# Performance work log

Measured on AMD Instinct MI355X. Metric: run time of the kernel, lower is better.

Reference implementation:

```python
import jax, jax.numpy as jnp
import numpy as np

NEG_INF = -1e9


def setup_inputs() -> dict:
    key = jax.random.key(0)
    ks = jax.random.split(key, 6)
    B, S, E, D = 32, 2048, 1024, 1024
    dec_hidden = jax.random.normal(ks[0], (B, D), dtype=jnp.float32)
    enc_outputs = jax.random.normal(ks[1], (B, S, E), dtype=jnp.float32)
    mask = jax.random.randint(ks[2], (B, S), 0, 2, dtype=jnp.int32)
    # scale weights ~ Glorot-ish so tanh isn't saturated
    W_enc = jax.random.normal(ks[3], (D, E), dtype=jnp.float32) / np.sqrt(E)
    W_dec = jax.random.normal(ks[4], (D, D), dtype=jnp.float32) / np.sqrt(D)
    v = jax.random.normal(ks[5], (D,), dtype=jnp.float32) / np.sqrt(D)
    return {"dec_hidden": dec_hidden, "enc_outputs": enc_outputs, "mask": mask,
            "W_enc": W_enc, "W_dec": W_dec, "v": v}


def reference(dec_hidden, enc_outputs, mask, W_enc, W_dec, v):
    # dh: [B, D]  (torch Linear: x @ W.T)
    dh = dec_hidden @ W_dec.T
    # eh: [B, S, D]
    eh = jnp.einsum('bse,de->bsd', enc_outputs, W_enc)
    # additive energy + projection by v -> scores [B, S]
    energy = jnp.tanh(dh[:, None, :] + eh)
    scores = jnp.einsum('bsd,d->bs', energy, v)
    scores = jnp.where(mask == 0, NEG_INF, scores)
    weights = jax.nn.softmax(scores, axis=1)          # [B, S]
    context = jnp.einsum('bs,bse->be', weights, enc_outputs)  # [B, E]
    return context, weights
```

## Files before the change

### kernel.cpp

```cpp
#include <hip/hip_runtime.h>
#include <stdint.h>

typedef float f32x4 __attribute__((ext_vector_type(4)));
typedef float f32x16 __attribute__((ext_vector_type(16)));
typedef short bf16x8 __attribute__((ext_vector_type(8)));
typedef unsigned short ushort8 __attribute__((ext_vector_type(8)));

__device__ __forceinline__ unsigned short f2bf(float x) {
  union { float f; uint32_t u; } c; c.f = x;
  return (unsigned short)((c.u + 0x8000u) >> 16);
}
__device__ __forceinline__ float bf2f(unsigned short u) {
  union { uint32_t u; float f; } c; c.u = ((uint32_t)u) << 16;
  return c.f;
}


__global__ void prep_fused_k(const float* __restrict__ W, unsigned short* __restrict__ Wt,
                             const float* __restrict__ dec, const float* __restrict__ Wd,
                             float* __restrict__ dh) {
  if (blockIdx.x < 512) {
    int t = blockIdx.x * 256 + threadIdx.x;
    int d  = t >> 7;
    int c0 = (t & 127) << 3;
    const float* src = W + ((size_t)d << 10) + c0;
    f32x4 f0 = *(const f32x4*)src;
    f32x4 f1 = *(const f32x4*)(src + 4);
    ushort8 u;
    u[0]=f2bf(f0[0]); u[1]=f2bf(f0[1]); u[2]=f2bf(f0[2]); u[3]=f2bf(f0[3]);
    u[4]=f2bf(f1[0]); u[5]=f2bf(f1[1]); u[6]=f2bf(f1[2]); u[7]=f2bf(f1[3]);
    int nt = d >> 7, r = d & 127;
    int kt = c0 >> 6, kb = (c0 & 63) >> 3;
    *(ushort8*)(Wt + ((size_t)nt << 17) + (kt << 13) + ((kb * 128 + r) << 3)) = u;
  } else {
    __shared__ float sdec[1024];
    int bb = blockIdx.x - 512;
    int b = bb >> 2;
    for (int i = threadIdx.x; i < 1024; i += 256) sdec[i] = dec[(b << 10) + i];
    __syncthreads();
    int d = ((bb & 3) << 8) + threadIdx.x;
    const float* wr = Wd + ((size_t)d << 10);
    float a = 0.f;
    for (int k = 0; k < 1024; k += 4) {
      f32x4 wv = *(const f32x4*)(wr + k);
      f32x4 xv = *(const f32x4*)(&sdec[k]);
      a += wv[0]*xv[0] + wv[1]*xv[1] + wv[2]*xv[2] + wv[3]*xv[3];
    }
    dh[(b << 10) + d] = a;
  }
}

__global__ void compact_k(const int* __restrict__ mask, int* __restrict__ rows,
                          int* __restrict__ cnt, float* __restrict__ wout) {
  int b = blockIdx.x, tid = threadIdx.x;
  int lane = tid & 63, wv = tid >> 6;
  int mloc[8]; int c = 0;
  #pragma unroll
  for (int ii = 0; ii < 8; ++ii) {
    int s = tid * 8 + ii;
    int m = mask[(b << 11) + s];
    mloc[ii] = m; c += m;
    wout[(b << 11) + s] = 0.f;
  }
  int inc = c;
  #pragma unroll
  for (int off = 1; off < 64; off <<= 1) {
    int nn = __shfl_up(inc, off);
    if (lane >= off) inc += nn;
  }
  __shared__ int wsum[4];
  if (lane == 63) wsum[wv] = inc;
  __syncthreads();
  int base = 0;
  for (int w = 0; w < wv; ++w) base += wsum[w];
  int idx = base + inc - c;
  #pragma unroll
  for (int ii = 0; ii < 8; ++ii) {
    if (mloc[ii]) { rows[(b << 11) + idx] = tid * 8 + ii; ++idx; }
  }
  if (tid == 0) cnt[b] = wsum[0] + wsum[1] + wsum[2] + wsum[3];
}

__global__ void pack8_k(const float* __restrict__ enc, const int* __restrict__ rows,
                        const int* __restrict__ cnt, unsigned short* __restrict__ encP) {
  int b = blockIdx.x >> 4, mt = blockIdx.x & 15;
  int n = cnt[b];
  if (mt * 128 >= n) return;
  __shared__ int sr[128];
  __shared__ unsigned short T[128 * 64];
  int tid = threadIdx.x;
  if (tid < 128) {
    int i = mt * 128 + tid; if (i >= n) i = n - 1;
    sr[tid] = rows[(b << 11) + i];
  }
  __syncthreads();
  unsigned short* dst = encP + (((size_t)(b * 16 + mt)) << 17);
  for (int kt = 0; kt < 16; ++kt) {
    #pragma unroll
    for (int p = 0; p < 4; ++p) {
      int id = p * 256 + tid;
      int r = id >> 3, cseg = id & 7;
      const float* src = enc + (((size_t)(b << 11) + sr[r]) << 10) + (kt << 6) + (cseg << 3);
      f32x4 f0 = *(const f32x4*)src;
      f32x4 f1 = *(const f32x4*)(src + 4);
      ushort8 u;
      u[0]=f2bf(f0[0]); u[1]=f2bf(f0[1]); u[2]=f2bf(f0[2]); u[3]=f2bf(f0[3]);
      u[4]=f2bf(f1[0]); u[5]=f2bf(f1[1]); u[6]=f2bf(f1[2]); u[7]=f2bf(f1[3]);
      *(ushort8*)&T[(r << 6) + ((cseg ^ (r & 7)) << 3)] = u;
    }
    __syncthreads();
    unsigned short* g = dst + (kt << 13);
    #pragma unroll
    for (int p = 0; p < 4; ++p) {
      int blk = p * 256 + tid;
      int kb = blk >> 7, r = blk & 127;
      ushort8 u = *(const ushort8*)&T[(r << 6) + ((kb ^ (r & 7)) << 3)];
      *(ushort8*)(g + (blk << 3)) = u;
    }
    __syncthreads();
  }
}

__global__ __launch_bounds__(256, 4) void score9_k(
    const unsigned short* __restrict__ encP, const unsigned short* __restrict__ Wt,
    const float* __restrict__ dh, const float* __restrict__ v,
    const int* __restrict__ cnt, float* __restrict__ pscores)
{
  int L  = (blockIdx.x & 7) * 512 + (blockIdx.x >> 3);
  int b  = L >> 7, mt = (L >> 3) & 15, nt = L & 7;
  int n  = cnt[b];
  if (mt * 128 >= n) return;

  __shared__ __align__(16) unsigned short AS[2][4096];
  __shared__ __align__(16) unsigned short BS[2][4096];

  int tid  = threadIdx.x;
  int lane = tid & 63;
  int wv   = tid >> 6;
  int wm = wv >> 1, wn = wv & 1;
  int l31 = lane & 31, l5 = lane >> 5;

  const unsigned short* aT = encP + (((size_t)(b * 16 + mt)) << 17);
  const unsigned short* bT = Wt + ((size_t)nt << 17);

  int offA[2][2], offB[2][2];
  #pragma unroll
  for (int mf = 0; mf < 2; ++mf) {
    int r = wm * 64 + mf * 32 + l31;
    #pragma unroll
    for (int ki = 0; ki < 2; ++ki)
      offA[mf][ki] = (((ki * 2 + l5) << 7) + r) << 3;
  }
  #pragma unroll
  for (int nf = 0; nf < 2; ++nf) {
    int r = wn * 64 + nf * 32 + l31;
    #pragma unroll
    for (int ki = 0; ki < 2; ++ki)
      offB[nf][ki] = (((ki * 2 + l5) << 7) + r) << 3;
  }

  f32x16 acc[2][2];
  #pragma unroll
  for (int i = 0; i < 2; ++i)
    #pragma unroll
    for (int j = 0; j < 2; ++j)
      #pragma unroll
      for (int e = 0; e < 16; ++e)
        acc[i][j][e] = 0.f;

  auto stage = [&](int slot, int kt) {
    #pragma unroll
    for (int j = 0; j < 2; ++j) {
      int off = j * 2048 + tid * 8;
      __builtin_amdgcn_global_load_lds(
        (const __attribute__((address_space(1))) void*)(const void*)(aT + ((size_t)kt << 12) + off),
        (__attribute__((address_space(3))) void*)(void*)(&AS[slot][off]), 16, 0, 0);
      __builtin_amdgcn_global_load_lds(
        (const __attribute__((address_space(1))) void*)(const void*)(bT + ((size_t)kt << 12) + off),
        (__attribute__((address_space(3))) void*)(void*)(&BS[slot][off]), 16, 0, 0);
    }
  };

  auto compute = [&](int slot) {
    #pragma unroll
    for (int ki = 0; ki < 2; ++ki) {
      bf16x8 af[2], bf[2];
      #pragma unroll
      for (int mf = 0; mf < 2; ++mf) af[mf] = *(const bf16x8*)&AS[slot][offA[mf][ki]];
      #pragma unroll
      for (int nf = 0; nf < 2; ++nf) bf[nf] = *(const bf16x8*)&BS[slot][offB[nf][ki]];
      #pragma unroll
      for (int mf = 0; mf < 2; ++mf)
        #pragma unroll
        for (int nf = 0; nf < 2; ++nf)
          acc[mf][nf] = __builtin_amdgcn_mfma_f32_32x32x16_bf16(af[mf], bf[nf], acc[mf][nf], 0, 0, 0);
    }
  };

  stage(0, 0);
  __syncthreads();
  int slot = 0;
  for (int kt = 0; kt < 31; ++kt) {
    stage(slot ^ 1, kt + 1);
    compute(slot);
    __syncthreads();
    slot ^= 1;
  }
  compute(slot);

  float* sc = (float*)AS;
  float vv[2], dd[2];
  #pragma unroll
  for (int nf = 0; nf < 2; ++nf) {
    int dcol = nt * 128 + wn * 64 + nf * 32 + l31;
    vv[nf] = v[dcol];
    dd[nf] = dh[(b << 10) + dcol];
  }
  #pragma unroll
  for (int mf = 0; mf < 2; ++mf) {
    #pragma unroll
    for (int reg = 0; reg < 16; ++reg) {
      float p = 0.f;
      #pragma unroll
      for (int nf = 0; nf < 2; ++nf) {
        float x = acc[mf][nf][reg] + dd[nf];
        float e = __expf(2.0f * x);
        float t = 1.0f - __fdividef(2.0f, e + 1.0f);
        p += vv[nf] * t;
      }
      p += __shfl_xor(p, 1); p += __shfl_xor(p, 2); p += __shfl_xor(p, 4);
      p += __shfl_xor(p, 8); p += __shfl_xor(p, 16);
      if (l31 == 0) {
        int row = wm * 64 + mf * 32 + (reg & 3) + 8 * (reg >> 2) + 4 * l5;
        sc[row * 2 + wn] = p;
      }
    }
  }
  __syncthreads();
  if (tid < 128) {
    int i = mt * 128 + tid;
    if (i < n)
      pscores[(((size_t)nt) << 16) + (b << 11) + i] = sc[tid * 2 + 0] + sc[tid * 2 + 1];
  }
}

__global__ void softmax4_k(const float* __restrict__ ps, const int* __restrict__ rows,
                           const int* __restrict__ cnt, float* __restrict__ wout,
                           float* __restrict__ wc) {
  int b = blockIdx.x;
  int tid = threadIdx.x;
  int n = cnt[b];
  float val[8];
  float m = -INFINITY;
  #pragma unroll
  for (int ii = 0; ii < 8; ++ii) {
    int i = tid + ii * 256;
    float s = -INFINITY;
    if (i < n) {
      s = 0.f;
      #pragma unroll
      for (int nt = 0; nt < 8; ++nt) s += ps[(((size_t)nt) << 16) + (b << 11) + i];
    }
    val[ii] = s;
    m = fmaxf(m, s);
  }
  #pragma unroll
  for (int off = 1; off < 64; off <<= 1) m = fmaxf(m, __shfl_xor(m, off));
  __shared__ float r1[4], r2[4];
  if ((tid & 63) == 0) r1[tid >> 6] = m;
  __syncthreads();
  m = fmaxf(fmaxf(r1[0], r1[1]), fmaxf(r1[2], r1[3]));
  float ssum = 0.f;
  #pragma unroll
  for (int ii = 0; ii < 8; ++ii) { val[ii] = __expf(val[ii] - m); ssum += val[ii]; }
  #pragma unroll
  for (int off = 1; off < 64; off <<= 1) ssum += __shfl_xor(ssum, off);
  if ((tid & 63) == 0) r2[tid >> 6] = ssum;
  __syncthreads();
  ssum = r2[0] + r2[1] + r2[2] + r2[3];
  float inv = 1.0f / ssum;
  #pragma unroll
  for (int ii = 0; ii < 8; ++ii) {
    int i = tid + ii * 256;
    if (i < n) {
      float w = val[ii] * inv;
      wc[(b << 11) + i] = w;
      wout[((size_t)b << 11) + rows[(b << 11) + i]] = w;
    }
  }
}

__global__ void ctx8_k(const unsigned short* __restrict__ encP, const float* __restrict__ wc,
                       const int* __restrict__ cnt, float* __restrict__ cp) {
  int b = blockIdx.x >> 4, mt = blockIdx.x & 15;
  int n = cnt[b];
  float* out = cp + (((size_t)(b * 16 + mt)) << 10);
  int tid = threadIdx.x;
  if (mt * 128 >= n) {
    #pragma unroll
    for (int j = 0; j < 4; ++j) out[tid * 4 + j] = 0.f;
    return;
  }
  __shared__ float sw[128];
  __shared__ float red[128][8];
  if (tid < 128) {
    int i = mt * 128 + tid;
    sw[tid] = (i < n) ? wc[(b << 11) + i] : 0.f;
  }
  __syncthreads();
  const unsigned short* tile = encP + (((size_t)(b * 16 + mt)) << 17);
  int cb8  = tid & 127;
  int half = tid >> 7;
  const unsigned short* base = tile + ((cb8 >> 3) << 13) + ((cb8 & 7) << 10);
  float a[8];
  #pragma unroll
  for (int j = 0; j < 8; ++j) a[j] = 0.f;
  for (int rr = 0; rr < 64; ++rr) {
    int r = half * 64 + rr;
    float w = sw[r];
    ushort8 u = *(const ushort8*)(base + (r << 3));
    #pragma unroll
    for (int j = 0; j < 8; ++j) a[j] += w * bf2f(u[j]);
  }
  if (half == 1) {
    #pragma unroll
    for (int j = 0; j < 8; ++j) red[cb8][j] = a[j];
  }
  __syncthreads();
  if (half == 0) {
    #pragma unroll
    for (int j = 0; j < 8; ++j) out[cb8 * 8 + j] = a[j] + red[cb8][j];
  }
}

__global__ void ctx_red4_k(const float* __restrict__ cp, float* __restrict__ out) {
  int t = blockIdx.x * 256 + threadIdx.x;
  int b = t >> 10, e = t & 1023;
  float a = 0.f;
  #pragma unroll
  for (int mt = 0; mt < 16; ++mt) a += cp[(((size_t)(b * 16 + mt)) << 10) + e];
  out[t] = a;
}

extern "C" void kernel_launch(void* const* d_in, const int* in_sizes, int n_in,
                              void* d_out, int out_size, void* d_ws, size_t ws_size,
                              hipStream_t stream) {
  const float* dec  = (const float*)d_in[0];
  const float* enc  = (const float*)d_in[1];
  const int*   mask = (const int*)d_in[2];
  const float* Wenc = (const float*)d_in[3];
  const float* Wdec = (const float*)d_in[4];
  const float* v    = (const float*)d_in[5];
  float* out_ctx = (float*)d_out;
  float* out_w   = (float*)d_out + 32768;

  char* ws = (char*)d_ws;
  unsigned short* Wt = (unsigned short*)ws;
  float* dh    = (float*)(ws + (2u << 20));
  int*   rows  = (int*)(ws + (2u << 20) + (128u << 10));
  float* wc    = (float*)(ws + (2u << 20) + (384u << 10));
  int*   cnt   = (int*)(ws + (2u << 20) + (640u << 10));
  float* pscores = (float*)(ws + (3u << 20));
  float* cp      = (float*)(ws + (5u << 20));
  unsigned short* encP = (unsigned short*)(ws + (8ull << 20));

  hipLaunchKernelGGL(prep_fused_k, dim3(640),  dim3(256), 0, stream, Wenc, Wt, dec, Wdec, dh);
  hipLaunchKernelGGL(compact_k,    dim3(32),   dim3(256), 0, stream, mask, rows, cnt, out_w);
  hipLaunchKernelGGL(pack8_k,      dim3(512),  dim3(256), 0, stream, enc, rows, cnt, encP);
  hipLaunchKernelGGL(score9_k,     dim3(4096), dim3(256), 0, stream, encP, Wt, dh, v, cnt, pscores);
  hipLaunchKernelGGL(softmax4_k,   dim3(32),   dim3(256), 0, stream, pscores, rows, cnt, out_w, wc);
  hipLaunchKernelGGL(ctx8_k,       dim3(512),  dim3(256), 0, stream, encP, wc, cnt, cp);
  hipLaunchKernelGGL(ctx_red4_k,   dim3(128),  dim3(256), 0, stream, cp, out_ctx);
}
```

Before: 209.9 us.

## Triple-buffer score GEMM LDS with one barrier per k-step and manual waitcnts

Switches the score kernel's global-to-LDS staging from double to triple buffering. Each k-step now reads its fragments into registers, issues the prefetch two stages ahead, waits only on the older loads, and takes a single barrier before the MFMAs. The goal is to hide global load latency and drop the trailing barrier per iteration. In exchange LDS use rises to 48 KB per block and occupancy is lowered from 4 to 3 blocks, and correctness now depends on the hand-placed vmcnt and lgkmcnt waits.

```diff
diff --git a/kernel.cpp b/kernel.cpp
--- a/kernel.cpp
+++ b/kernel.cpp
@@ -121,7 +121,7 @@
   }
 }
 
-__global__ __launch_bounds__(256, 4) void score9_k(
+__global__ __launch_bounds__(256, 3) void score10_k(
     const unsigned short* __restrict__ encP, const unsigned short* __restrict__ Wt,
     const float* __restrict__ dh, const float* __restrict__ v,
     const int* __restrict__ cnt, float* __restrict__ pscores)
@@ -131,8 +131,8 @@
   int n  = cnt[b];
   if (mt * 128 >= n) return;
 
-  __shared__ __align__(16) unsigned short AS[2][4096];
-  __shared__ __align__(16) unsigned short BS[2][4096];
+  __shared__ __align__(16) unsigned short AS[3][4096];
+  __shared__ __align__(16) unsigned short BS[3][4096];
 
   int tid  = threadIdx.x;
   int lane = tid & 63;
@@ -181,33 +181,96 @@
     }
   };
 
-  auto compute = [&](int slot) {
-    #pragma unroll
-    for (int ki = 0; ki < 2; ++ki) {
-      bf16x8 af[2], bf[2];
-      #pragma unroll
-      for (int mf = 0; mf < 2; ++mf) af[mf] = *(const bf16x8*)&AS[slot][offA[mf][ki]];
-      #pragma unroll
-      for (int nf = 0; nf < 2; ++nf) bf[nf] = *(const bf16x8*)&BS[slot][offB[nf][ki]];
+#define VMFENCE(N) { asm volatile("s_waitcnt vmcnt(" #N ")" ::: "memory"); \
+                     __builtin_amdgcn_sched_barrier(0); }
+#define LKFENCE    { asm volatile("s_waitcnt lgkmcnt(0)" ::: "memory"); \
+                     __builtin_amdgcn_sched_barrier(0); }
+#define BARRIER    { __builtin_amdgcn_s_barrier(); __builtin_amdgcn_sched_barrier(0); }
+
+#define KBODY(SLOT, T, SSLOT)                                              \
+  {                                                                        \
+    bf16x8 af[2][2], bf[2][2];                                             \
+    _Pragma("unroll")                                                      \
+    for (int mf = 0; mf < 2; ++mf)                                         \
+      _Pragma("unroll")                                                    \
+      for (int ki = 0; ki < 2; ++ki)                                       \
+        af[mf][ki] = *(const bf16x8*)&AS[SLOT][offA[mf][ki]];              \
+    _Pragma("unroll")                                                      \
+    for (int nf = 0; nf < 2; ++nf)                                         \
+      _Pragma("unroll")                                                    \
+      for (int ki = 0; ki < 2; ++ki)                                       \
+        bf[nf][ki] = *(const bf16x8*)&BS[SLOT][offB[nf][ki]];              \
+    LKFENCE                                                                \
+    stage((SSLOT), (T) + 2);                                               \
+    VMFENCE(4)                                                             \
+    BARRIER                                                                \
+    _Pragma("unroll")                                                      \
+    for (int ki = 0; ki < 2; ++ki)                                         \
+      _Pragma("unroll")                                                    \
+      for (int mf = 0; mf < 2; ++mf)                                       \
+        _Pragma("unroll")                                                  \
+        for (int nf = 0; nf < 2; ++nf)                                     \
+          acc[mf][nf] = __builtin_amdgcn_mfma_f32_32x32x16_bf16(           \
+              af[mf][ki], bf[nf][ki], acc[mf][nf], 0, 0, 0);               \
+  }
+
+  stage(0, 0);
+  stage(1, 1);
+  VMFENCE(4)
+  BARRIER
+
+  #pragma unroll 1
+  for (int t = 0; t < 30; t += 3) {
+    KBODY(0, t,     2)
+    KBODY(1, t + 1, 0)
+    KBODY(2, t + 2, 1)
+  }
+  {
+    bf16x8 af[2][2], bf[2][2];
+    #pragma unroll
+    for (int mf = 0; mf < 2; ++mf)
+      #pragma unroll
+      for (int ki = 0; ki < 2; ++ki)
+        af[mf][ki] = *(const bf16x8*)&AS[0][offA[mf][ki]];
+    #pragma unroll
+    for (int nf = 0; nf < 2; ++nf)
+      #pragma unroll
+      for (int ki = 0; ki < 2; ++ki)
+        bf[nf][ki] = *(const bf16x8*)&BS[0][offB[nf][ki]];
+    LKFENCE
+    VMFENCE(0)
+    BARRIER
+    #pragma unroll
+    for (int ki = 0; ki < 2; ++ki)
       #pragma unroll
       for (int mf = 0; mf < 2; ++mf)
         #pragma unroll
         for (int nf = 0; nf < 2; ++nf)
-          acc[mf][nf] = __builtin_amdgcn_mfma_f32_32x32x16_bf16(af[mf], bf[nf], acc[mf][nf], 0, 0, 0);
-    }
-  };
-
-  stage(0, 0);
-  __syncthreads();
-  int slot = 0;
-  for (int kt = 0; kt < 31; ++kt) {
-    stage(slot ^ 1, kt + 1);
-    compute(slot);
-    __syncthreads();
-    slot ^= 1;
-  }
-  compute(slot);
-
+          acc[mf][nf] = __builtin_amdgcn_mfma_f32_32x32x16_bf16(af[mf][ki], bf[nf][ki], acc[mf][nf], 0, 0, 0);
+  }
+  {
+    bf16x8 af[2][2], bf[2][2];
+    #pragma unroll
+    for (int mf = 0; mf < 2; ++mf)
+      #pragma unroll
+      for (int ki = 0; ki < 2; ++ki)
+        af[mf][ki] = *(const bf16x8*)&AS[1][offA[mf][ki]];
+    #pragma unroll
+    for (int nf = 0; nf < 2; ++nf)
+      #pragma unroll
+      for (int ki = 0; ki < 2; ++ki)
+        bf[nf][ki] = *(const bf16x8*)&BS[1][offB[nf][ki]];
+    #pragma unroll
+    for (int ki = 0; ki < 2; ++ki)
+      #pragma unroll
+      for (int mf = 0; mf < 2; ++mf)
+        #pragma unroll
+        for (int nf = 0; nf < 2; ++nf)
+          acc[mf][nf] = __builtin_amdgcn_mfma_f32_32x32x16_bf16(af[mf][ki], bf[nf][ki], acc[mf][nf], 0, 0, 0);
+  }
+#undef KBODY
+
+  __syncthreads();
   float* sc = (float*)AS;
   float vv[2], dd[2];
   #pragma unroll
@@ -367,7 +430,7 @@
   hipLaunchKernelGGL(prep_fused_k, dim3(640),  dim3(256), 0, stream, Wenc, Wt, dec, Wdec, dh);
   hipLaunchKernelGGL(compact_k,    dim3(32),   dim3(256), 0, stream, mask, rows, cnt, out_w);
   hipLaunchKernelGGL(pack8_k,      dim3(512),  dim3(256), 0, stream, enc, rows, cnt, encP);
-  hipLaunchKernelGGL(score9_k,     dim3(4096), dim3(256), 0, stream, encP, Wt, dh, v, cnt, pscores);
+  hipLaunchKernelGGL(score10_k,    dim3(4096), dim3(256), 0, stream, encP, Wt, dh, v, cnt, pscores);
   hipLaunchKernelGGL(softmax4_k,   dim3(32),   dim3(256), 0, stream, pscores, rows, cnt, out_w, wc);
   hipLaunchKernelGGL(ctx8_k,       dim3(512),  dim3(256), 0, stream, encP, wc, cnt, cp);
   hipLaunchKernelGGL(ctx_red4_k,   dim3(128),  dim3(256), 0, stream, cp, out_ctx);
```

Result: faster. 198.8 us (-5.3%).

## Triple-buffer score GEMM with explicit waitcnt fences and fuse compaction into prep

Applied to the files above, without the earlier changes.

The score GEMM moves from a double-buffered LDS pipeline to a three-stage one. It uses manual vmcnt/lgkmcnt waits and raw barriers, so global loads run two tiles ahead of compute. Occupancy is lowered from 4 to 3 blocks per CU to make room for the extra LDS. Separately, the mask compaction kernel is folded into the prep kernel as extra blocks, which removes one launch. The risks are less latency hiding from the lower occupancy, and fragile hand-placed wait counts that assume a fixed number of outstanding loads per stage.

```diff
diff --git a/kernel.cpp b/kernel.cpp
--- a/kernel.cpp
+++ b/kernel.cpp
@@ -18,7 +18,9 @@
 
 __global__ void prep_fused_k(const float* __restrict__ W, unsigned short* __restrict__ Wt,
                              const float* __restrict__ dec, const float* __restrict__ Wd,
-                             float* __restrict__ dh) {
+                             float* __restrict__ dh, const int* __restrict__ mask,
+                             int* __restrict__ rows, int* __restrict__ cnt,
+                             float* __restrict__ wout) {
   if (blockIdx.x < 512) {
     int t = blockIdx.x * 256 + threadIdx.x;
     int d  = t >> 7;
@@ -32,7 +34,7 @@
     int nt = d >> 7, r = d & 127;
     int kt = c0 >> 6, kb = (c0 & 63) >> 3;
     *(ushort8*)(Wt + ((size_t)nt << 17) + (kt << 13) + ((kb * 128 + r) << 3)) = u;
-  } else {
+  } else if (blockIdx.x < 640) {
     __shared__ float sdec[1024];
     int bb = blockIdx.x - 512;
     int b = bb >> 2;
@@ -47,38 +49,35 @@
       a += wv[0]*xv[0] + wv[1]*xv[1] + wv[2]*xv[2] + wv[3]*xv[3];
     }
     dh[(b << 10) + d] = a;
-  }
-}
-
-__global__ void compact_k(const int* __restrict__ mask, int* __restrict__ rows,
-                          int* __restrict__ cnt, float* __restrict__ wout) {
-  int b = blockIdx.x, tid = threadIdx.x;
-  int lane = tid & 63, wv = tid >> 6;
-  int mloc[8]; int c = 0;
-  #pragma unroll
-  for (int ii = 0; ii < 8; ++ii) {
-    int s = tid * 8 + ii;
-    int m = mask[(b << 11) + s];
-    mloc[ii] = m; c += m;
-    wout[(b << 11) + s] = 0.f;
-  }
-  int inc = c;
-  #pragma unroll
-  for (int off = 1; off < 64; off <<= 1) {
-    int nn = __shfl_up(inc, off);
-    if (lane >= off) inc += nn;
-  }
-  __shared__ int wsum[4];
-  if (lane == 63) wsum[wv] = inc;
-  __syncthreads();
-  int base = 0;
-  for (int w = 0; w < wv; ++w) base += wsum[w];
-  int idx = base + inc - c;
-  #pragma unroll
-  for (int ii = 0; ii < 8; ++ii) {
-    if (mloc[ii]) { rows[(b << 11) + idx] = tid * 8 + ii; ++idx; }
-  }
-  if (tid == 0) cnt[b] = wsum[0] + wsum[1] + wsum[2] + wsum[3];
+  } else {
+    int b = blockIdx.x - 640, tid = threadIdx.x;
+    int lane = tid & 63, wvx = tid >> 6;
+    int mloc[8]; int c = 0;
+    #pragma unroll
+    for (int ii = 0; ii < 8; ++ii) {
+      int s = tid * 8 + ii;
+      int m = mask[(b << 11) + s];
+      mloc[ii] = m; c += m;
+      wout[(b << 11) + s] = 0.f;
+    }
+    int inc = c;
+    #pragma unroll
+    for (int off = 1; off < 64; off <<= 1) {
+      int nn = __shfl_up(inc, off);
+      if (lane >= off) inc += nn;
+    }
+    __shared__ int wsum[4];
+    if (lane == 63) wsum[wvx] = inc;
+    __syncthreads();
+    int base = 0;
+    for (int w = 0; w < wvx; ++w) base += wsum[w];
+    int idx = base + inc - c;
+    #pragma unroll
+    for (int ii = 0; ii < 8; ++ii) {
+      if (mloc[ii]) { rows[(b << 11) + idx] = tid * 8 + ii; ++idx; }
+    }
+    if (tid == 0) cnt[b] = wsum[0] + wsum[1] + wsum[2] + wsum[3];
+  }
 }
 
 __global__ void pack8_k(const float* __restrict__ enc, const int* __restrict__ rows,
@@ -121,7 +120,7 @@
   }
 }
 
-__global__ __launch_bounds__(256, 4) void score9_k(
+__global__ __launch_bounds__(256, 3) void score11_k(
     const unsigned short* __restrict__ encP, const unsigned short* __restrict__ Wt,
     const float* __restrict__ dh, const float* __restrict__ v,
     const int* __restrict__ cnt, float* __restrict__ pscores)
@@ -131,8 +130,8 @@
   int n  = cnt[b];
   if (mt * 128 >= n) return;
 
-  __shared__ __align__(16) unsigned short AS[2][4096];
-  __shared__ __align__(16) unsigned short BS[2][4096];
+  __shared__ __align__(16) unsigned short AS[3][4096];
+  __shared__ __align__(16) unsigned short BS[3][4096];
 
   int tid  = threadIdx.x;
   int lane = tid & 63;
@@ -197,17 +196,34 @@
     }
   };
 
+#define VMFENCE(N) { asm volatile("s_waitcnt vmcnt(" #N ")" ::: "memory"); \
+                     __builtin_amdgcn_sched_barrier(0); }
+#define LKFENCE    { asm volatile("s_waitcnt lgkmcnt(0)" ::: "memory"); \
+                     __builtin_amdgcn_sched_barrier(0); }
+#define BARRIER    { __builtin_amdgcn_s_barrier(); __builtin_amdgcn_sched_barrier(0); }
+
+#define KBODY(SLOT, T, SSLOT)  \
+  { stage((SSLOT), (T) + 2); compute(SLOT); LKFENCE VMFENCE(4) BARRIER }
+
   stage(0, 0);
-  __syncthreads();
-  int slot = 0;
-  for (int kt = 0; kt < 31; ++kt) {
-    stage(slot ^ 1, kt + 1);
-    compute(slot);
-    __syncthreads();
-    slot ^= 1;
-  }
-  compute(slot);
-
+  stage(1, 1);
+  VMFENCE(4)
+  BARRIER
+
+  #pragma unroll 1
+  for (int t = 0; t < 30; t += 3) {
+    KBODY(0, t,     2)
+    KBODY(1, t + 1, 0)
+    KBODY(2, t + 2, 1)
+  }
+#undef KBODY
+  compute(0);
+  LKFENCE
+  VMFENCE(0)
+  BARRIER
+  compute(1);
+
+  __syncthreads();
   float* sc = (float*)AS;
   float vv[2], dd[2];
   #pragma unroll
@@ -364,10 +380,10 @@
   float* cp      = (float*)(ws + (5u << 20));
   unsigned short* encP = (unsigned short*)(ws + (8ull << 20));
 
-  hipLaunchKernelGGL(prep_fused_k, dim3(640),  dim3(256), 0, stream, Wenc, Wt, dec, Wdec, dh);
-  hipLaunchKernelGGL(compact_k,    dim3(32),   dim3(256), 0, stream, mask, rows, cnt, out_w);
+  hipLaunchKernelGGL(prep_fused_k, dim3(672),  dim3(256), 0, stream, Wenc, Wt, dec, Wdec, dh,
+                     mask, rows, cnt, out_w);
   hipLaunchKernelGGL(pack8_k,      dim3(512),  dim3(256), 0, stream, enc, rows, cnt, encP);
-  hipLaunchKernelGGL(score9_k,     dim3(4096), dim3(256), 0, stream, encP, Wt, dh, v, cnt, pscores);
+  hipLaunchKernelGGL(score11_k,    dim3(4096), dim3(256), 0, stream, encP, Wt, dh, v, cnt, pscores);
   hipLaunchKernelGGL(softmax4_k,   dim3(32),   dim3(256), 0, stream, pscores, rows, cnt, out_w, wc);
   hipLaunchKernelGGL(ctx8_k,       dim3(512),  dim3(256), 0, stream, encP, wc, cnt, cp);
   hipLaunchKernelGGL(ctx_red4_k,   dim3(128),  dim3(256), 0, stream, cp, out_ctx);
```

After: 201.9 us. 1.04x faster.
